# Performance work log

Measured on AMD Instinct MI355X. Metric: run time of the kernel, lower is better.

Reference implementation:

```python
import jax, jax.numpy as jnp
import numpy as np

B, T, C, H = 2, 2048, 1024, 16
HD = C // H

def setup_inputs() -> dict:
    key = jax.random.key(0)
    ks = jax.random.split(key, 5)
    x = jax.random.normal(ks[0], (B, T, C), dtype=jnp.float32)
    # causal mask, broadcast over batch and heads
    mask = jnp.tril(jnp.ones((T, T), dtype=jnp.int32))[None, None]
    scale = 0.02
    qkv_w = jax.random.normal(ks[1], (3 * C, C), dtype=jnp.float32) * scale
    qkv_b = jax.random.normal(ks[2], (3 * C,), dtype=jnp.float32) * scale
    out_w = jax.random.normal(ks[3], (C, C), dtype=jnp.float32) * scale
    out_b = jax.random.normal(ks[4], (C,), dtype=jnp.float32) * scale
    return {"x": x, "mask": mask, "qkv_w": qkv_w, "qkv_b": qkv_b,
            "out_w": out_w, "out_b": out_b}

def reference(x, mask, qkv_w, qkv_b, out_w, out_b):
    b, t, c = x.shape
    # torch Linear: y = x @ W^T + b
    qkv = jnp.einsum('btc,oc->bto', x, qkv_w) + qkv_b  # [B,T,3C]
    q, k, v = jnp.split(qkv, 3, axis=-1)
    def heads(u):
        return u.reshape(b, t, H, HD).transpose(0, 2, 1, 3)  # [B,H,T,HD]
    q, k, v = heads(q), heads(k), heads(v)
    attn = jnp.einsum('bhqd,bhkd->bhqk', q, k) / jnp.sqrt(jnp.float32(HD))
    attn = jnp.where(mask == 0, jnp.float32(-jnp.inf), attn)
    attn = jax.nn.softmax(attn, axis=-1)
    out = jnp.einsum('bhqk,bhkd->bhqd', attn, v)
    out = out.transpose(0, 2, 1, 3).reshape(b, t, c)
    return jnp.einsum('btc,oc->bto', out, out_w) + out_b
```

## Files before the change

### kernel.cpp

```cpp
#include <hip/hip_runtime.h>
#include <hip/hip_bf16.h>
#include <math.h>

#define B_  2
#define T_  2048
#define C_  1024
#define H_  16
#define HD_ 64

typedef __attribute__((ext_vector_type(8))) short short8;
typedef __attribute__((ext_vector_type(4))) float floatx4;

__device__ __forceinline__ short f2bf(float f) {
    __hip_bfloat16 h = __float2bfloat16(f);
    return *reinterpret_cast<short*>(&h);
}

__device__ __forceinline__ float fexp2(float x) {
#if __has_builtin(__builtin_amdgcn_exp2f)
    return __builtin_amdgcn_exp2f(x);
#else
    return exp2f(x);
#endif
}

__device__ __forceinline__ unsigned pack2bf(float a, float b) {
    return __builtin_amdgcn_perm(__float_as_uint(b), __float_as_uint(a),
                                 0x07060302u);
}

__device__ __forceinline__ void gld16(const void* g, void* l) {
    __builtin_amdgcn_global_load_lds(
        (const __attribute__((address_space(1))) void*)g,
        (__attribute__((address_space(3))) void*)l, 16, 0, 0);
}

__global__ __launch_bounds__(256)
void cast3(const float* __restrict__ x, const float* __restrict__ w1,
           const float* __restrict__ w2, short* __restrict__ xo,
           short* __restrict__ w1o, short* __restrict__ w2o)
{
    int gid = blockIdx.x * 256 + threadIdx.x;
    const float* s; short* d; int off;
    if (gid < 524288)      { s = x;  d = xo;  off = gid; }
    else if (gid < 917504) { s = w1; d = w1o; off = gid - 524288; }
    else                   { s = w2; d = w2o; off = gid - 917504; }
    float4 a = ((const float4*)s)[(size_t)off * 2];
    float4 b = ((const float4*)s)[(size_t)off * 2 + 1];
    short8 v;
    v[0] = f2bf(a.x); v[1] = f2bf(a.y); v[2] = f2bf(a.z); v[3] = f2bf(a.w);
    v[4] = f2bf(b.x); v[5] = f2bf(b.y); v[6] = f2bf(b.z); v[7] = f2bf(b.w);
    *(short8*)(d + (size_t)off * 8) = v;
}

template<int MODE, int BM, int BN, int BK>
__global__ __launch_bounds__(256, 4)
void gemm_bf16(const short* __restrict__ A, const short* __restrict__ W,
               const float* __restrict__ bias, float* __restrict__ out,
               short* __restrict__ qb, short* __restrict__ kb,
               short* __restrict__ vt, int M, int N, int K)
{
    constexpr int MI  = BM / 32;
    constexpr int NJ  = BN / 32;
    constexpr int KS  = BK / 32;
    constexpr int CPR = BK / 8;
    constexpr int LC  = (CPR == 8) ? 3 : 4;
    constexpr int RPT = 256 / CPR;
    __shared__ __align__(16) short As[2][BM * BK];
    __shared__ __align__(16) short Bs[2][BN * BK];

    const int tid  = threadIdx.x;
    const int lane = tid & 63;
    const int w    = tid >> 6;
    const int m    = lane & 15, quad = lane >> 4;
    const int wrow = w >> 1, wcol = w & 1;
    const int nb = blockIdx.x, mb = blockIdx.y;

    const int g = (tid & (CPR - 1)) ^ ((tid >> LC) & (CPR - 1));
    const short* Ag = A + (size_t)(mb * BM + (tid >> LC)) * K + g * 8;
    const short* Wg = W + (size_t)(nb * BN + (tid >> LC)) * K + g * 8;

    int aoff[MI][KS], boff[NJ][KS];
#pragma unroll
    for (int i = 0; i < MI; i++) {
        int ar = wrow * (BM / 2) + i * 16 + m;
#pragma unroll
        for (int ks = 0; ks < KS; ks++)
            aoff[i][ks] = ar * BK + (((ks * 4 + quad) ^ (ar & (CPR - 1))) * 8);
    }
#pragma unroll
    for (int j = 0; j < NJ; j++) {
        int bc = wcol * (BN / 2) + j * 16 + m;
#pragma unroll
        for (int ks = 0; ks < KS; ks++)
            boff[j][ks] = bc * BK + (((ks * 4 + quad) ^ (bc & (CPR - 1))) * 8);
    }

    floatx4 acc[MI][NJ];
#pragma unroll
    for (int i = 0; i < MI; i++)
#pragma unroll
        for (int j = 0; j < NJ; j++) acc[i][j] = (floatx4){0.f, 0.f, 0.f, 0.f};

    auto stage = [&](int k0, int bi) {
#pragma unroll
        for (int i = 0; i < BM / RPT; i++)
            gld16(Ag + (size_t)(i * RPT) * K + k0, As[bi] + i * 2048 + tid * 8);
#pragma unroll
        for (int i = 0; i < BN / RPT; i++)
            gld16(Wg + (size_t)(i * RPT) * K + k0, Bs[bi] + i * 2048 + tid * 8);
    };

    const int nk = K / BK;
    stage(0, 0);
    __syncthreads();

    for (int ki = 0; ki < nk; ki++) {
        const int cur = ki & 1;
        if (ki + 1 < nk) stage((ki + 1) * BK, cur ^ 1);

        const short* Ac = &As[cur][0];
        const short* Bc = &Bs[cur][0];
        short8 af[MI][KS], bfr[NJ][KS];
#pragma unroll
        for (int i = 0; i < MI; i++)
#pragma unroll
            for (int ks = 0; ks < KS; ks++)
                af[i][ks] = *(const short8*)(Ac + aoff[i][ks]);
#pragma unroll
        for (int j = 0; j < NJ; j++)
#pragma unroll
            for (int ks = 0; ks < KS; ks++)
                bfr[j][ks] = *(const short8*)(Bc + boff[j][ks]);
#pragma unroll
        for (int i = 0; i < MI; i++)
#pragma unroll
            for (int j = 0; j < NJ; j++)
#pragma unroll
                for (int ks = 0; ks < KS; ks++)
                    acc[i][j] = __builtin_amdgcn_mfma_f32_16x16x32_bf16(
                        af[i][ks], bfr[j][ks], acc[i][j], 0, 0, 0);
        __syncthreads();
    }

    const int row0 = mb * BM + wrow * (BM / 2);
    const int col0 = nb * BN + wcol * (BN / 2);

    if (MODE == 0) {
#pragma unroll
        for (int j = 0; j < NJ; j++) {
            int n = col0 + j * 16 + m;
            float bn = bias[n];
#pragma unroll
            for (int i = 0; i < MI; i++) {
#pragma unroll
                for (int r = 0; r < 4; r++) {
                    int mm = row0 + i * 16 + quad * 4 + r;
                    out[(size_t)mm * N + n] = acc[i][j][r] + bn;
                }
            }
        }
    } else {
        const int sec = col0 >> 10;
        const int h   = (col0 >> 6) & 15;
        if (sec <= 1) {
            short* dst = sec ? kb : qb;
            const float sc = sec ? 1.0f : 0.18033688011112042f;
#pragma unroll
            for (int j = 0; j < NJ; j++) {
                int n = col0 + j * 16 + m;
                int d = n & 63;
                float bn = bias[n];
#pragma unroll
                for (int i = 0; i < MI; i++) {
                    int t0 = row0 + i * 16 + quad * 4;
                    int b  = t0 >> 11;
                    int t  = t0 & (T_ - 1);
#pragma unroll
                    for (int r = 0; r < 4; r++)
                        dst[((size_t)(b * H_ + h) * T_ + t + r) * HD_ + d] =
                            f2bf((acc[i][j][r] + bn) * sc);
                }
            }
        } else {
#pragma unroll
            for (int j = 0; j < NJ; j++) {
                int n = col0 + j * 16 + m;
                int d = n & 63;
                float bn = bias[n];
#pragma unroll
                for (int i = 0; i < MI; i++) {
                    int t0 = row0 + i * 16 + quad * 4;
                    int b  = t0 >> 11;
                    int t  = t0 & (T_ - 1);
                    ushort4 u;
                    u.x = (unsigned short)f2bf(acc[i][j][0] + bn);
                    u.y = (unsigned short)f2bf(acc[i][j][1] + bn);
                    u.z = (unsigned short)f2bf(acc[i][j][2] + bn);
                    u.w = (unsigned short)f2bf(acc[i][j][3] + bn);
                    *(ushort4*)(vt + ((size_t)(b * H_ + h) * HD_ + d) * T_ + t) = u;
                }
            }
        }
    }
}

__global__ __launch_bounds__(256, 2)
void attn_mfma(const short* __restrict__ qb, const short* __restrict__ kb,
               const short* __restrict__ vt, short* __restrict__ ao)
{
    __shared__ __align__(16) short Ks[2][64 * 64];
    __shared__ __align__(16) short Vs[2][64 * 64];
    __shared__ __align__(16) short Ps[8][16 * 64];

    const int tid  = threadIdx.x;
    const int w    = tid >> 6;
    const int lane = tid & 63;
    const int m    = lane & 15;
    const int quad = lane >> 4;

    const int bid = blockIdx.x;
    const int bh  = ((bid & 7) << 2) | ((bid >> 3) & 3);
    const int qt  = 15 - (bid >> 5);
    const int b   = bh >> 4, h = bh & 15;

    int off8[8];
#pragma unroll
    for (int ks = 0; ks < 2; ks++)
#pragma unroll
        for (int nt = 0; nt < 4; nt++)
            off8[ks * 4 + nt] = (nt * 16 + m) * 64 + (((quad + 4 * ks) ^ (m & 7)) * 8);

    short* Ps0 = &Ps[w * 2 + 0][0];
    short* Ps1 = &Ps[w * 2 + 1][0];
    int pw[4], pr[2];
#pragma unroll
    for (int nt = 0; nt < 4; nt++)
        pw[nt] = m * 64 + (((2 * nt + (quad >> 1)) ^ (m & 7)) * 8) + (quad & 1) * 4;
#pragma unroll
    for (int ks = 0; ks < 2; ks++)
        pr[ks] = m * 64 + (((4 * ks + quad) ^ (m & 7)) * 8);

    const short* kbh = kb + (size_t)bh * T_ * HD_;
    const short* vbh = vt + (size_t)bh * HD_ * T_;

    const short* qp0 = qb + ((size_t)bh * T_ + qt * 128 + w * 32 + m) * HD_;
    const short* qp1 = qp0 + 16 * HD_;
    short8 qa0 = *(const short8*)(qp0 + quad * 8);
    short8 qa1 = *(const short8*)(qp0 + quad * 8 + 32);
    short8 qc0 = *(const short8*)(qp1 + quad * 8);
    short8 qc1 = *(const short8*)(qp1 + quad * 8 + 32);

    auto stage = [&](int kt2, int bi) {
        const int kbase = kt2 * 64;
#pragma unroll
        for (int it = 0; it < 2; it++) {
            int ci = it * 256 + tid;
            int rr = ci >> 3, cp = ci & 7, c = cp ^ (rr & 7);
            gld16(kbh + ((size_t)(kbase + rr)) * HD_ + c * 8, Ks[bi] + ci * 8);
            gld16(vbh + (size_t)rr * T_ + kbase + c * 8, Vs[bi] + ci * 8);
        }
    };

    const int NTL = 2 * qt + 2;

    stage(0, 0);
    __syncthreads();
    stage(1, 1);

    floatx4 o0[4], o1[4];
#pragma unroll
    for (int nt = 0; nt < 4; nt++) {
        o0[nt] = (floatx4){0.f, 0.f, 0.f, 0.f};
        o1[nt] = (floatx4){0.f, 0.f, 0.f, 0.f};
    }
    float lr0 = 0.f, lr1 = 0.f;

    for (int kt = 0; kt < NTL; kt++) {
        const int cur = kt & 1;
        const short* Kc = Ks[cur];
        const short* Vc = Vs[cur];

        short8 kf0[4], kf1[4];
#pragma unroll
        for (int nt = 0; nt < 4; nt++) {
            kf0[nt] = *(const short8*)(Kc + off8[nt]);
            kf1[nt] = *(const short8*)(Kc + off8[4 + nt]);
        }

        const int koff = (kt - 2 * qt) * 64;

        auto qk_sm = [&](short8 qA, short8 qB, short* PsS, int qloc, float& lr) {
            floatx4 s[4];
#pragma unroll
            for (int nt = 0; nt < 4; nt++) {
                floatx4 c = {0.f, 0.f, 0.f, 0.f};
                c = __builtin_amdgcn_mfma_f32_16x16x32_bf16(kf0[nt], qA, c, 0, 0, 0);
                c = __builtin_amdgcn_mfma_f32_16x16x32_bf16(kf1[nt], qB, c, 0, 0, 0);
                s[nt] = c;
            }
            if (kt >= 2 * qt) {
#pragma unroll
                for (int nt = 0; nt < 4; nt++)
#pragma unroll
                    for (int rr = 0; rr < 4; rr++)
                        if (koff + nt * 16 + quad * 4 + rr > qloc) s[nt][rr] = -1e30f;
            }
            float rs = 0.f;
#pragma unroll
            for (int nt = 0; nt < 4; nt++) {
#pragma unroll
                for (int rr = 0; rr < 4; rr++) {
                    float p = fexp2(s[nt][rr]);
                    rs += p;
                    s[nt][rr] = p;
                }
                uint2 pk;
                pk.x = pack2bf(s[nt][0], s[nt][1]);
                pk.y = pack2bf(s[nt][2], s[nt][3]);
                *(uint2*)(PsS + pw[nt]) = pk;
            }
            rs += __shfl_xor(rs, 16, 64);
            rs += __shfl_xor(rs, 32, 64);
            lr += rs;
        };
        qk_sm(qa0, qa1, Ps0, w * 32 + m,      lr0);
        qk_sm(qc0, qc1, Ps1, w * 32 + 16 + m, lr1);

        short8 p00 = *(const short8*)(Ps0 + pr[0]);
        short8 p01 = *(const short8*)(Ps0 + pr[1]);
        short8 p10 = *(const short8*)(Ps1 + pr[0]);
        short8 p11 = *(const short8*)(Ps1 + pr[1]);

#pragma unroll
        for (int nt = 0; nt < 4; nt++) {
            short8 v0 = *(const short8*)(Vc + off8[nt]);
            short8 v1 = *(const short8*)(Vc + off8[4 + nt]);
            o0[nt] = __builtin_amdgcn_mfma_f32_16x16x32_bf16(v0, p00, o0[nt], 0, 0, 0);
            o0[nt] = __builtin_amdgcn_mfma_f32_16x16x32_bf16(v1, p01, o0[nt], 0, 0, 0);
            o1[nt] = __builtin_amdgcn_mfma_f32_16x16x32_bf16(v0, p10, o1[nt], 0, 0, 0);
            o1[nt] = __builtin_amdgcn_mfma_f32_16x16x32_bf16(v1, p11, o1[nt], 0, 0, 0);
        }

        __syncthreads();
        if (kt + 2 < NTL) stage(kt + 2, cur);
    }

    const float inv0 = 1.0f / lr0;
    const float inv1 = 1.0f / lr1;
    const int q0 = qt * 128 + w * 32 + m;
    short* dst0 = ao + ((size_t)b * T_ + q0) * C_ + h * HD_;
    short* dst1 = dst0 + 16 * C_;
#pragma unroll
    for (int nt = 0; nt < 4; nt++) {
        ushort4 u;
        u.x = (unsigned short)f2bf(o0[nt][0] * inv0);
        u.y = (unsigned short)f2bf(o0[nt][1] * inv0);
        u.z = (unsigned short)f2bf(o0[nt][2] * inv0);
        u.w = (unsigned short)f2bf(o0[nt][3] * inv0);
        *(ushort4*)(dst0 + nt * 16 + quad * 4) = u;
        ushort4 u2;
        u2.x = (unsigned short)f2bf(o1[nt][0] * inv1);
        u2.y = (unsigned short)f2bf(o1[nt][1] * inv1);
        u2.z = (unsigned short)f2bf(o1[nt][2] * inv1);
        u2.w = (unsigned short)f2bf(o1[nt][3] * inv1);
        *(ushort4*)(dst1 + nt * 16 + quad * 4) = u2;
    }
}

extern "C" void kernel_launch(void* const* d_in, const int* in_sizes, int n_in,
                              void* d_out, int out_size, void* d_ws, size_t ws_size,
                              hipStream_t stream)
{
    const float* x     = (const float*)d_in[0];
    const float* qkv_w = (const float*)d_in[2];
    const float* qkv_b = (const float*)d_in[3];
    const float* out_w = (const float*)d_in[4];
    const float* out_b = (const float*)d_in[5];
    float* out = (float*)d_out;

    const size_t BTC = (size_t)B_ * T_ * C_;
    short* xb  = (short*)d_ws;
    short* w1b = xb  + BTC;
    short* w2b = w1b + 3 * (size_t)C_ * C_;
    short* qbw = w2b + (size_t)C_ * C_;
    short* kbw = qbw + BTC;
    short* vtw = kbw + BTC;
    short* aob = vtw + BTC;

    cast3<<<4096, 256, 0, stream>>>(x, qkv_w, out_w, xb, w1b, w2b);

    dim3 g1(3 * C_ / 64, B_ * T_ / 128);
    gemm_bf16<1, 128, 64, 64><<<g1, 256, 0, stream>>>(xb, w1b, qkv_b, nullptr,
                                                      qbw, kbw, vtw,
                                                      B_ * T_, 3 * C_, C_);

    attn_mfma<<<512, 256, 0, stream>>>(qbw, kbw, vtw, aob);

    dim3 g3(C_ / 64, B_ * T_ / 128);
    gemm_bf16<0, 128, 64, 64><<<g3, 256, 0, stream>>>(aob, w2b, out_b, out,
                                                      nullptr, nullptr, nullptr,
                                                      B_ * T_, C_, C_);
}
```

Before: 188.4 us.

## Pair complementary causal query tiles per block for balanced attention work

Each block now handles two 64-row query tiles, p and 31-p, instead of one contiguous 128-row tile. All blocks then do roughly equal work under the causal mask, which removes the tail imbalance where early tiles finish quickly and late tiles dominate. The second tile's QK and PV work is skipped once its diagonal is passed. This adds branches inside the loop, and K/V reuse per load drops for the short tile.

```diff
diff --git a/kernel.cpp b/kernel.cpp
--- a/kernel.cpp
+++ b/kernel.cpp
@@ -221,7 +221,9 @@
 
     const int bid = blockIdx.x;
     const int bh  = ((bid & 7) << 2) | ((bid >> 3) & 3);
-    const int qt  = 15 - (bid >> 5);
+    const int p   = (bid >> 5) & 15;
+    const int qA  = 31 - p;
+    const int qB  = p;
     const int b   = bh >> 4, h = bh & 15;
 
     int off8[8];
@@ -244,12 +246,12 @@
     const short* kbh = kb + (size_t)bh * T_ * HD_;
     const short* vbh = vt + (size_t)bh * HD_ * T_;
 
-    const short* qp0 = qb + ((size_t)bh * T_ + qt * 128 + w * 32 + m) * HD_;
-    const short* qp1 = qp0 + 16 * HD_;
-    short8 qa0 = *(const short8*)(qp0 + quad * 8);
-    short8 qa1 = *(const short8*)(qp0 + quad * 8 + 32);
-    short8 qc0 = *(const short8*)(qp1 + quad * 8);
-    short8 qc1 = *(const short8*)(qp1 + quad * 8 + 32);
+    const short* qpA = qb + ((size_t)bh * T_ + qA * 64 + w * 16 + m) * HD_;
+    const short* qpB = qb + ((size_t)bh * T_ + qB * 64 + w * 16 + m) * HD_;
+    short8 qa0 = *(const short8*)(qpA + quad * 8);
+    short8 qa1 = *(const short8*)(qpA + quad * 8 + 32);
+    short8 qc0 = *(const short8*)(qpB + quad * 8);
+    short8 qc1 = *(const short8*)(qpB + quad * 8 + 32);
 
     auto stage = [&](int kt2, int bi) {
         const int kbase = kt2 * 64;
@@ -262,7 +264,7 @@
         }
     };
 
-    const int NTL = 2 * qt + 2;
+    const int NTL = qA + 1;
 
     stage(0, 0);
     __syncthreads();
@@ -280,6 +282,7 @@
         const int cur = kt & 1;
         const short* Kc = Ks[cur];
         const short* Vc = Vs[cur];
+        const bool doB = (kt <= qB);
 
         short8 kf0[4], kf1[4];
 #pragma unroll
@@ -288,32 +291,30 @@
             kf1[nt] = *(const short8*)(Kc + off8[4 + nt]);
         }
 
-        const int koff = (kt - 2 * qt) * 64;
-
-        auto qk_sm = [&](short8 qA, short8 qB, short* PsS, int qloc, float& lr) {
+        auto qk_sm = [&](short8 qX, short8 qY, short* PsS, bool diag, float& lr) {
             floatx4 s[4];
 #pragma unroll
             for (int nt = 0; nt < 4; nt++) {
                 floatx4 c = {0.f, 0.f, 0.f, 0.f};
-                c = __builtin_amdgcn_mfma_f32_16x16x32_bf16(kf0[nt], qA, c, 0, 0, 0);
-                c = __builtin_amdgcn_mfma_f32_16x16x32_bf16(kf1[nt], qB, c, 0, 0, 0);
+                c = __builtin_amdgcn_mfma_f32_16x16x32_bf16(kf0[nt], qX, c, 0, 0, 0);
+                c = __builtin_amdgcn_mfma_f32_16x16x32_bf16(kf1[nt], qY, c, 0, 0, 0);
                 s[nt] = c;
             }
-            if (kt >= 2 * qt) {
+            if (diag) {
 #pragma unroll
                 for (int nt = 0; nt < 4; nt++)
 #pragma unroll
                     for (int rr = 0; rr < 4; rr++)
-                        if (koff + nt * 16 + quad * 4 + rr > qloc) s[nt][rr] = -1e30f;
+                        if (nt * 16 + quad * 4 + rr > w * 16 + m) s[nt][rr] = -1e30f;
             }
             float rs = 0.f;
 #pragma unroll
             for (int nt = 0; nt < 4; nt++) {
 #pragma unroll
                 for (int rr = 0; rr < 4; rr++) {
-                    float p = fexp2(s[nt][rr]);
-                    rs += p;
-                    s[nt][rr] = p;
+                    float pv = fexp2(s[nt][rr]);
+                    rs += pv;
+                    s[nt][rr] = pv;
                 }
                 uint2 pk;
                 pk.x = pack2bf(s[nt][0], s[nt][1]);
@@ -324,13 +325,11 @@
             rs += __shfl_xor(rs, 32, 64);
             lr += rs;
         };
-        qk_sm(qa0, qa1, Ps0, w * 32 + m,      lr0);
-        qk_sm(qc0, qc1, Ps1, w * 32 + 16 + m, lr1);
+        qk_sm(qa0, qa1, Ps0, kt == qA, lr0);
+        if (doB) qk_sm(qc0, qc1, Ps1, kt == qB, lr1);
 
         short8 p00 = *(const short8*)(Ps0 + pr[0]);
         short8 p01 = *(const short8*)(Ps0 + pr[1]);
-        short8 p10 = *(const short8*)(Ps1 + pr[0]);
-        short8 p11 = *(const short8*)(Ps1 + pr[1]);
 
 #pragma unroll
         for (int nt = 0; nt < 4; nt++) {
@@ -338,8 +337,17 @@
             short8 v1 = *(const short8*)(Vc + off8[4 + nt]);
             o0[nt] = __builtin_amdgcn_mfma_f32_16x16x32_bf16(v0, p00, o0[nt], 0, 0, 0);
             o0[nt] = __builtin_amdgcn_mfma_f32_16x16x32_bf16(v1, p01, o0[nt], 0, 0, 0);
-            o1[nt] = __builtin_amdgcn_mfma_f32_16x16x32_bf16(v0, p10, o1[nt], 0, 0, 0);
-            o1[nt] = __builtin_amdgcn_mfma_f32_16x16x32_bf16(v1, p11, o1[nt], 0, 0, 0);
+        }
+        if (doB) {
+            short8 p10 = *(const short8*)(Ps1 + pr[0]);
+            short8 p11 = *(const short8*)(Ps1 + pr[1]);
+#pragma unroll
+            for (int nt = 0; nt < 4; nt++) {
+                short8 v0 = *(const short8*)(Vc + off8[nt]);
+                short8 v1 = *(const short8*)(Vc + off8[4 + nt]);
+                o1[nt] = __builtin_amdgcn_mfma_f32_16x16x32_bf16(v0, p10, o1[nt], 0, 0, 0);
+                o1[nt] = __builtin_amdgcn_mfma_f32_16x16x32_bf16(v1, p11, o1[nt], 0, 0, 0);
+            }
         }
 
         __syncthreads();
@@ -348,9 +356,10 @@
 
     const float inv0 = 1.0f / lr0;
     const float inv1 = 1.0f / lr1;
-    const int q0 = qt * 128 + w * 32 + m;
-    short* dst0 = ao + ((size_t)b * T_ + q0) * C_ + h * HD_;
-    short* dst1 = dst0 + 16 * C_;
+    const int rA = qA * 64 + w * 16 + m;
+    const int rB = qB * 64 + w * 16 + m;
+    short* dst0 = ao + ((size_t)b * T_ + rA) * C_ + h * HD_;
+    short* dst1 = ao + ((size_t)b * T_ + rB) * C_ + h * HD_;
 #pragma unroll
     for (int nt = 0; nt < 4; nt++) {
         ushort4 u;
```

New measurement: 185.4 us. About the same (-1.6%).
